# Kernel optimization log

Hardware: AMD Instinct MI355X
Metric: run time of the kernel (lower is better)

## Reference

```python
import jax, jax.numpy as jnp
import numpy as np

N = 50000          # atoms (nodes)
NEIGH = 12         # neighbors per atom
N_CRYS = 500       # crystals, 100 atoms each (contiguous)
H_E = 128          # h_fea_edge
H_A = 128          # h_fea_angle
N_CLS = 2
BOND_STEPS, BOND_MIN, BOND_MAX = 40, 0.0, 8.0
ANG_STEPS, ANG_MIN, ANG_MAX = 8, -1.0, 1.0


def _gbf(data, dmin, dmax, steps):
    # Gaussian basis expansion on the last (new) axis
    filters = jnp.linspace(dmin, dmax, steps, dtype=jnp.float32)
    gamma = (dmax - dmin) / steps
    return jnp.exp(-((data[..., None] - filters) ** 2) / (gamma ** 2))


def _sage_conv(x, src, dst, Wl, Wr, b):
    # PyG SAGEConv, mean aggregation:
    #   out_i = Wl @ mean_{(j->i) in E} x_j + b + Wr @ x_i
    n = x.shape[0]
    msg = x[src]                                             # [E, F] gather
    agg = jax.ops.segment_sum(msg, dst, num_segments=n)      # [N, F] scatter-add
    cnt = jax.ops.segment_sum(jnp.ones((src.shape[0],), x.dtype), dst, num_segments=n)
    agg = agg / jnp.maximum(cnt, 1.0)[:, None]
    return agg @ Wl.T + b + x @ Wr.T


def _segment_mean_pool(x, crys_idx):
    # crys_idx: [C, 2] contiguous [start, end) ranges covering [0, N)
    n = x.shape[0]
    starts = crys_idx[:, 0]
    seg_id = jnp.searchsorted(starts, jnp.arange(n), side='right') - 1
    counts = (crys_idx[:, 1] - crys_idx[:, 0]).astype(x.dtype)
    summed = jax.ops.segment_sum(x, seg_id, num_segments=crys_idx.shape[0])
    return summed / jnp.maximum(counts, 1.0)[:, None]


def setup_inputs() -> dict:
    key = jax.random.key(0)
    ks = jax.random.split(key, 24)
    in_b = BOND_STEPS * NEIGH            # 480
    in_a = ANG_STEPS * NEIGH * NEIGH     # 1152
    h_cat = H_E + H_A                    # 256

    def lin(k, fo, fi):
        return jax.random.normal(k, (fo, fi), jnp.float32) * (1.0 / np.sqrt(fi))

    atoms_per = N // N_CRYS
    starts = np.arange(N_CRYS, dtype=np.int32) * atoms_per
    crys_idx = jnp.asarray(np.stack([starts, starts + atoms_per], axis=1))

    return {
        'bond_fea': jax.random.uniform(ks[0], (N, NEIGH), jnp.float32) * BOND_MAX,
        'angle_fea': jax.random.uniform(ks[1], (N, NEIGH, NEIGH), jnp.float32) * 2.0 - 1.0,
        'species': jax.random.randint(ks[2], (N,), 0, 100, jnp.int32),
        'nbr_idx': jax.random.randint(ks[3], (N, NEIGH), 0, N, jnp.int32),
        'crys_idx': crys_idx,
        'Wl_b1': lin(ks[4], H_E, in_b), 'Wr_b1': lin(ks[5], H_E, in_b),
        'b_b1': jnp.zeros((H_E,), jnp.float32),
        'Wl_a1': lin(ks[6], H_A, in_a), 'Wr_a1': lin(ks[7], H_A, in_a),
        'b_a1': jnp.zeros((H_A,), jnp.float32),
        'Wl_b': jnp.stack([lin(ks[8], H_E, H_E), lin(ks[9], H_E, H_E)]),
        'Wr_b': jnp.stack([lin(ks[10], H_E, H_E), lin(ks[11], H_E, H_E)]),
        'b_b': jnp.zeros((2, H_E), jnp.float32),
        'Wl_a': jnp.stack([lin(ks[12], H_A, H_A), lin(ks[13], H_A, H_A)]),
        'Wr_a': jnp.stack([lin(ks[14], H_A, H_A), lin(ks[15], H_A, H_A)]),
        'b_a': jnp.zeros((2, H_A), jnp.float32),
        'W_mlp': jnp.stack([lin(ks[16], h_cat, h_cat), lin(ks[17], h_cat, h_cat)]),
        'b_mlp': jnp.zeros((2, h_cat), jnp.float32),
        'W_fc': lin(ks[18], N_CLS, h_cat),
        'b_fc': jnp.zeros((N_CLS,), jnp.float32),
    }


def reference(bond_fea, angle_fea, species, nbr_idx, crys_idx,
              Wl_b1, Wr_b1, b_b1, Wl_a1, Wr_a1, b_a1,
              Wl_b, Wr_b, b_b, Wl_a, Wr_a, b_a,
              W_mlp, b_mlp, W_fc, b_fc):
    n, neigh = nbr_idx.shape
    # get_edge_index: source = repeated node id, dest = neighbor id
    src = jnp.repeat(jnp.arange(n, dtype=nbr_idx.dtype), neigh)   # [N*neigh]
    dst = nbr_idx.reshape(-1)                                     # [N*neigh]

    # GBF expansions, flattened per node
    edge_fea = _gbf(bond_fea, BOND_MIN, BOND_MAX, BOND_STEPS).reshape(n, -1)    # [N, 480]
    ang_fea = _gbf(angle_fea, ANG_MIN, ANG_MAX, ANG_STEPS).reshape(n, -1)       # [N, 1152]

    # first SAGE layers (dropout_prob = 0 -> identity)
    b_out = jax.nn.relu(_sage_conv(edge_fea, src, dst, Wl_b1, Wr_b1, b_b1))
    a_out = jax.nn.relu(_sage_conv(ang_fea, src, dst, Wl_a1, Wr_a1, b_a1))

    # stacked SAGE layers (n_conv - 1 = 2 each)
    for i in range(Wl_b.shape[0]):
        b_out = jax.nn.relu(_sage_conv(b_out, src, dst, Wl_b[i], Wr_b[i], b_b[i]))
    for i in range(Wl_a.shape[0]):
        a_out = jax.nn.relu(_sage_conv(a_out, src, dst, Wl_a[i], Wr_a[i], b_a[i]))

    crys_fea = jnp.concatenate([b_out, a_out], axis=1)   # [N, 256]
    crys_fea = _segment_mean_pool(crys_fea, crys_idx)     # [C, 256]

    for i in range(W_mlp.shape[0]):
        crys_fea = crys_fea @ W_mlp[i].T + b_mlp[i]

    return crys_fea @ W_fc.T + b_fc                       # [C, n_classification]
```

## Files before the change

kernel.cpp:

```cpp
#include <hip/hip_runtime.h>

typedef _Float16 f16;
typedef _Float16 f16x8 __attribute__((ext_vector_type(8)));
typedef float f32x4 __attribute__((ext_vector_type(4)));

#define N_ATOMS 50000
#define NEIGH   12
#define NEDGE   (N_ATOMS * NEIGH)
#define NCRYS   500
#define NBLK    196

template <int MODE, int K>
__global__ __launch_bounds__(512) void gemm1(
    const float* __restrict__ Asrc, const f16* __restrict__ Wcat,
    f16* __restrict__ P, f16* __restrict__ Q, int n) {
  __shared__ __align__(16) f16 As[2][4][128][8];
  const int tid = threadIdx.x;
  const int lane = tid & 63;
  const int wid = tid >> 6;
  const int wr = wid >> 2;
  const int wc = wid & 3;
  const int row0 = blockIdx.x * 128;
  const int r16 = lane & 15;
  const int kb = lane >> 4;

  const int sAkb = tid & 3;
  const int sArow = tid >> 2;
  int arow = row0 + sArow;
  if (arow >= n) arow = n - 1;

  const f16* wb[4];
#pragma unroll
  for (int q = 0; q < 4; ++q)
    wb[q] = Wcat + (size_t)(wc * 64 + q * 16 + r16) * K + kb * 8;

  constexpr float G2I = (MODE == 1) ? 25.0f : 16.0f;
  constexpr float DLT = (MODE == 1) ? (8.0f / 39.0f) : (2.0f / 7.0f);
  constexpr float C1 = 2.0f * G2I * DLT;
  constexpr float C2 = G2I * DLT * DLT;
  const float S = __expf(-2.0f * C2);
  constexpr int RUN = (MODE == 1) ? 4 : 8;

  f32x4 acc[4][4];
#pragma unroll
  for (int m = 0; m < 4; ++m)
#pragma unroll
    for (int q = 0; q < 4; ++q) acc[m][q] = (f32x4)0.f;

  auto stageA = [&](int buf, int t) {
    int kg0 = t * 32 + sAkb * 8;
    int jn, kk0;
    if constexpr (MODE == 1) {
      jn = kg0 / 40;
      kk0 = kg0 - jn * 40;
    } else {
      jn = kg0 >> 3;
      kk0 = 0;
    }
    float d = Asrc[(size_t)arow * (MODE == 1 ? 12 : 144) + jn];
    f16 v[8];
#pragma unroll
    for (int h = 0; h < 8 / RUN; ++h) {
      float f0 = (float)(kk0 + h * RUN) * DLT + (MODE == 2 ? -1.0f : 0.0f);
      float u = d - f0;
      float g = __expf(-G2I * u * u);
      float ratio = __expf(C1 * u - C2);
      v[h * RUN] = (f16)g;
#pragma unroll
      for (int j = 1; j < RUN; ++j) {
        g *= ratio;
        ratio *= S;
        v[h * RUN + j] = (f16)g;
      }
    }
    *(f16x8*)&As[buf][sAkb][sArow][0] = *(const f16x8*)v;
  };

  constexpr int NT = K / 32;
  f16x8 bcur[4], bnxt[4];
  stageA(0, 0);
#pragma unroll
  for (int q = 0; q < 4; ++q) bcur[q] = *(const f16x8*)(wb[q]);
  __syncthreads();
  int buf = 0;
  for (int t = 0; t < NT; ++t) {
    if (t + 1 < NT) {
      stageA(buf ^ 1, t + 1);
#pragma unroll
      for (int q = 0; q < 4; ++q) bnxt[q] = *(const f16x8*)(wb[q] + (t + 1) * 32);
    }
    f16x8 a[4];
#pragma unroll
    for (int m = 0; m < 4; ++m)
      a[m] = *(const f16x8*)&As[buf][kb][wr * 64 + m * 16 + r16][0];
#pragma unroll
    for (int m = 0; m < 4; ++m)
#pragma unroll
      for (int q = 0; q < 4; ++q)
        acc[m][q] =
            __builtin_amdgcn_mfma_f32_16x16x32_f16(a[m], bcur[q], acc[m][q], 0, 0, 0);
    __syncthreads();
#pragma unroll
    for (int q = 0; q < 4; ++q) bcur[q] = bnxt[q];
    buf ^= 1;
  }

  const int crow = (lane >> 4) * 4;
  const int ccol = lane & 15;
  f16* outp = (wc < 2) ? P : Q;
  const int cbase = (wc & 1) * 64;
#pragma unroll
  for (int m = 0; m < 4; ++m) {
#pragma unroll
    for (int r = 0; r < 4; ++r) {
      int row = row0 + wr * 64 + m * 16 + crow + r;
      if (row < n) {
#pragma unroll
        for (int q = 0; q < 4; ++q)
          outp[(size_t)row * 128 + cbase + q * 16 + ccol] = (f16)acc[m][q][r];
      }
    }
  }
}

__global__ __launch_bounds__(256) void gemmL_reg(
    const f16* __restrict__ srcB, const f16* __restrict__ srcA,
    f16* __restrict__ dstB, f16* __restrict__ dstA, const f16* __restrict__ Wall,
    const float* __restrict__ bb, const float* __restrict__ ba, int lidx, int n) {
  const int path = blockIdx.y;
  const f16* src = path ? srcA : srcB;
  f16* dst = path ? dstA : dstB;
  const f16* W = Wall + (size_t)(path * 2 + lidx) * 32768;
  const float* bias = (path ? ba : bb) + lidx * 128;

  const int lane = threadIdx.x & 63;
  const int wid = threadIdx.x >> 6;
  const int wr = wid & 1;
  const int wc = wid >> 1;
  const int row0 = blockIdx.x * 128;
  const int r16 = lane & 15;
  const int kb = lane >> 4;

  int rm[4];
#pragma unroll
  for (int m = 0; m < 4; ++m) {
    int r = row0 + wr * 64 + m * 16 + r16;
    rm[m] = (r < n) ? r : (n - 1);
  }
  const f16* wb[4];
#pragma unroll
  for (int q = 0; q < 4; ++q)
    wb[q] = W + (size_t)(wc * 64 + q * 16 + r16) * 256 + kb * 8;

  f32x4 acc[4][4];
#pragma unroll
  for (int m = 0; m < 4; ++m)
#pragma unroll
    for (int q = 0; q < 4; ++q) acc[m][q] = (f32x4)0.f;

#pragma unroll
  for (int t = 0; t < 8; ++t) {
    f16x8 a[4], b[4];
#pragma unroll
    for (int m = 0; m < 4; ++m)
      a[m] = *(const f16x8*)&src[(size_t)rm[m] * 256 + t * 32 + kb * 8];
#pragma unroll
    for (int q = 0; q < 4; ++q) b[q] = *(const f16x8*)(wb[q] + t * 32);
#pragma unroll
    for (int m = 0; m < 4; ++m)
#pragma unroll
      for (int q = 0; q < 4; ++q)
        acc[m][q] =
            __builtin_amdgcn_mfma_f32_16x16x32_f16(a[m], b[q], acc[m][q], 0, 0, 0);
  }

  const int crow = (lane >> 4) * 4;
  const int ccol = lane & 15;
#pragma unroll
  for (int m = 0; m < 4; ++m) {
#pragma unroll
    for (int r = 0; r < 4; ++r) {
      int row = row0 + wr * 64 + m * 16 + crow + r;
      if (row < n) {
#pragma unroll
        for (int q = 0; q < 4; ++q) {
          int col = wc * 64 + q * 16 + ccol;
          float v = acc[m][q][r] + bias[col];
          dst[(size_t)row * 256 + 128 + col] = (f16)fmaxf(v, 0.0f);
        }
      }
    }
  }
}

__global__ void cvtW(const float* __restrict__ Wl, const float* __restrict__ Wr,
                     f16* __restrict__ outp, int K) {
  int c = blockIdx.y;
  int k = blockIdx.x * 256 + threadIdx.x;
  if (k < K)
    outp[(size_t)c * K + k] =
        (f16)((c < 128) ? Wl[(size_t)c * K + k] : Wr[(size_t)(c - 128) * K + k]);
}

__global__ void cvtW_small(const float* __restrict__ Wl_b, const float* __restrict__ Wr_b,
                           const float* __restrict__ Wl_a, const float* __restrict__ Wr_a,
                           f16* __restrict__ outp) {
  int idx = blockIdx.x * 256 + threadIdx.x;
  int l = idx >> 15;
  int c = (idx >> 8) & 127;
  int k = idx & 255;
  const float* Wl = (l < 2) ? Wl_b + (size_t)l * 16384 : Wl_a + (size_t)(l - 2) * 16384;
  const float* Wr = (l < 2) ? Wr_b + (size_t)l * 16384 : Wr_a + (size_t)(l - 2) * 16384;
  float v = (k < 128) ? Wl[(size_t)c * 128 + k] : Wr[(size_t)c * 128 + (k - 128)];
  outp[idx] = (f16)v;
}

__global__ void k_count(const int* __restrict__ nbr, int* __restrict__ deg) {
  int e = blockIdx.x * 256 + threadIdx.x;
  if (e < NEDGE) atomicAdd(&deg[nbr[e]], 1);
}
__global__ void k_scan1(const int* __restrict__ deg, int* __restrict__ rowptr,
                        int* __restrict__ bsum) {
  __shared__ int s[256];
  int t = threadIdx.x, i = blockIdx.x * 256 + t;
  int v = (i < N_ATOMS) ? deg[i] : 0;
  s[t] = v;
  __syncthreads();
  for (int off = 1; off < 256; off <<= 1) {
    int x = (t >= off) ? s[t - off] : 0;
    __syncthreads();
    s[t] += x;
    __syncthreads();
  }
  if (i < N_ATOMS) rowptr[i] = s[t] - v;
  if (t == 255) bsum[blockIdx.x] = s[255];
}
__global__ void k_scan2(int* __restrict__ bsum) {
  __shared__ int s[256];
  int t = threadIdx.x;
  int v = (t < NBLK) ? bsum[t] : 0;
  s[t] = v;
  __syncthreads();
  for (int off = 1; off < 256; off <<= 1) {
    int x = (t >= off) ? s[t - off] : 0;
    __syncthreads();
    s[t] += x;
    __syncthreads();
  }
  if (t < NBLK) bsum[t] = s[t] - v;
}
__global__ void k_scan3(int* __restrict__ rowptr, const int* __restrict__ bsum) {
  int i = blockIdx.x * 256 + threadIdx.x;
  if (i < N_ATOMS) rowptr[i] += bsum[blockIdx.x];
  if (i == 0) rowptr[N_ATOMS] = NEDGE;
}
__global__ void k_fill(const int* __restrict__ nbr, const int* __restrict__ rowptr,
                       int* __restrict__ cursor, int* __restrict__ eidx) {
  int e = blockIdx.x * 256 + threadIdx.x;
  if (e < NEDGE) {
    int dst = nbr[e];
    int pos = rowptr[dst] + atomicAdd(&cursor[dst], 1);
    eidx[pos] = e / NEIGH;
  }
}

__global__ __launch_bounds__(256) void gather_fin1(
    const f16* __restrict__ Pb, const f16* __restrict__ Qb,
    const f16* __restrict__ Pa, const f16* __restrict__ Qa,
    const int* __restrict__ rowptr, const int* __restrict__ eidx,
    const float* __restrict__ bias_b, const float* __restrict__ bias_a,
    f16* __restrict__ axb, f16* __restrict__ axa) {
  const int path = blockIdx.y;
  const f16* P = path ? Pa : Pb;
  const f16* Q = path ? Qa : Qb;
  const float* bias = path ? bias_a : bias_b;
  f16* ax = path ? axa : axb;
  const int t = threadIdx.x;
  const int a = blockIdx.x * 16 + (t >> 4);
  const int g = (t & 15) * 8;
  const int s0 = rowptr[a], s1 = rowptr[a + 1];
  float acc[8];
#pragma unroll
  for (int u = 0; u < 8; ++u) acc[u] = 0.f;
  int j = s0;
  for (; j + 8 <= s1; j += 8) {
    int e[8];
#pragma unroll
    for (int u = 0; u < 8; ++u) e[u] = eidx[j + u];
    f16x8 v[8];
#pragma unroll
    for (int u = 0; u < 8; ++u) v[u] = *(const f16x8*)&P[(size_t)e[u] * 128 + g];
#pragma unroll
    for (int u = 0; u < 8; ++u)
#pragma unroll
      for (int c = 0; c < 8; ++c) acc[c] += (float)v[u][c];
  }
  for (; j + 4 <= s1; j += 4) {
    int e0 = eidx[j], e1 = eidx[j + 1], e2 = eidx[j + 2], e3 = eidx[j + 3];
    f16x8 v0 = *(const f16x8*)&P[(size_t)e0 * 128 + g];
    f16x8 v1 = *(const f16x8*)&P[(size_t)e1 * 128 + g];
    f16x8 v2 = *(const f16x8*)&P[(size_t)e2 * 128 + g];
    f16x8 v3 = *(const f16x8*)&P[(size_t)e3 * 128 + g];
#pragma unroll
    for (int c = 0; c < 8; ++c)
      acc[c] += ((float)v0[c] + (float)v1[c]) + ((float)v2[c] + (float)v3[c]);
  }
  for (; j < s1; ++j) {
    f16x8 v = *(const f16x8*)&P[(size_t)eidx[j] * 128 + g];
#pragma unroll
    for (int c = 0; c < 8; ++c) acc[c] += (float)v[c];
  }
  f16x8 q = *(const f16x8*)&Q[(size_t)a * 128 + g];
  float inv = 1.0f / fmaxf((float)(s1 - s0), 1.0f);
  f16 outv[8];
#pragma unroll
  for (int u = 0; u < 8; ++u) {
    float v = acc[u] * inv + bias[g + u] + (float)q[u];
    outv[u] = (f16)fmaxf(v, 0.0f);
  }
  *(f16x8*)&ax[(size_t)a * 256 + 128 + g] = *(const f16x8*)outv;
}

__global__ __launch_bounds__(256) void gather_mean(
    f16* __restrict__ axb, f16* __restrict__ axa,
    const int* __restrict__ rowptr, const int* __restrict__ eidx) {
  f16* ax = blockIdx.y ? axa : axb;
  const int t = threadIdx.x;
  const int a = blockIdx.x * 16 + (t >> 4);
  const int g = (t & 15) * 8;
  const int s0 = rowptr[a], s1 = rowptr[a + 1];
  float acc[8];
#pragma unroll
  for (int u = 0; u < 8; ++u) acc[u] = 0.f;
  int j = s0;
  for (; j + 8 <= s1; j += 8) {
    int e[8];
#pragma unroll
    for (int u = 0; u < 8; ++u) e[u] = eidx[j + u];
    f16x8 v[8];
#pragma unroll
    for (int u = 0; u < 8; ++u)
      v[u] = *(const f16x8*)&ax[(size_t)e[u] * 256 + 128 + g];
#pragma unroll
    for (int u = 0; u < 8; ++u)
#pragma unroll
      for (int c = 0; c < 8; ++c) acc[c] += (float)v[u][c];
  }
  for (; j + 4 <= s1; j += 4) {
    int e0 = eidx[j], e1 = eidx[j + 1], e2 = eidx[j + 2], e3 = eidx[j + 3];
    f16x8 v0 = *(const f16x8*)&ax[(size_t)e0 * 256 + 128 + g];
    f16x8 v1 = *(const f16x8*)&ax[(size_t)e1 * 256 + 128 + g];
    f16x8 v2 = *(const f16x8*)&ax[(size_t)e2 * 256 + 128 + g];
    f16x8 v3 = *(const f16x8*)&ax[(size_t)e3 * 256 + 128 + g];
#pragma unroll
    for (int c = 0; c < 8; ++c)
      acc[c] += ((float)v0[c] + (float)v1[c]) + ((float)v2[c] + (float)v3[c]);
  }
  for (; j < s1; ++j) {
    f16x8 v = *(const f16x8*)&ax[(size_t)eidx[j] * 256 + 128 + g];
#pragma unroll
    for (int c = 0; c < 8; ++c) acc[c] += (float)v[c];
  }
  float inv = 1.0f / fmaxf((float)(s1 - s0), 1.0f);
  f16 outv[8];
#pragma unroll
  for (int u = 0; u < 8; ++u) outv[u] = (f16)(acc[u] * inv);
  *(f16x8*)&ax[(size_t)a * 256 + g] = *(const f16x8*)outv;
}

__global__ __launch_bounds__(256) void head_kernel(
    const f16* __restrict__ axb, const f16* __restrict__ axa,
    const int* __restrict__ crys, const float* __restrict__ W_mlp,
    const float* __restrict__ b_mlp, const float* __restrict__ W_fc,
    const float* __restrict__ b_fc, float* __restrict__ outp) {
  __shared__ float sh0[256], sh1[256];
  const int cry = blockIdx.x, c = threadIdx.x;
  const int s = crys[2 * cry], e = crys[2 * cry + 1];
  const f16* src = (c < 128) ? axb : axa;
  const int ch = c & 127;
  float sum = 0.f;
  for (int r = s; r < e; ++r) sum += (float)src[(size_t)r * 256 + 128 + ch];
  sh0[c] = sum / fmaxf((float)(e - s), 1.0f);
  __syncthreads();
  {
    const float* wrow = W_mlp + (size_t)c * 256;
    float s2 = b_mlp[c];
#pragma unroll 8
    for (int k = 0; k < 256; k += 4) {
      float4 w = *(const float4*)&wrow[k];
      s2 += sh0[k] * w.x + sh0[k + 1] * w.y + sh0[k + 2] * w.z + sh0[k + 3] * w.w;
    }
    sh1[c] = s2;
  }
  __syncthreads();
  {
    const float* wrow = W_mlp + 65536 + (size_t)c * 256;
    float s2 = b_mlp[256 + c];
#pragma unroll 8
    for (int k = 0; k < 256; k += 4) {
      float4 w = *(const float4*)&wrow[k];
      s2 += sh1[k] * w.x + sh1[k + 1] * w.y + sh1[k + 2] * w.z + sh1[k + 3] * w.w;
    }
    sh0[c] = s2;
  }
  __syncthreads();
  if (c < 2) {
    const float* wrow = W_fc + c * 256;
    float s2 = b_fc[c];
    for (int k = 0; k < 256; ++k) s2 += sh0[k] * wrow[k];
    outp[cry * 2 + c] = s2;
  }
}

extern "C" void kernel_launch(void* const* d_in, const int* in_sizes, int n_in,
                              void* d_out, int out_size, void* d_ws, size_t ws_size,
                              hipStream_t stream) {
  const float* bond  = (const float*)d_in[0];
  const float* angle = (const float*)d_in[1];
  const int*   nbr   = (const int*)d_in[3];
  const int*   crys  = (const int*)d_in[4];
  const float* Wl_b1 = (const float*)d_in[5];
  const float* Wr_b1 = (const float*)d_in[6];
  const float* b_b1  = (const float*)d_in[7];
  const float* Wl_a1 = (const float*)d_in[8];
  const float* Wr_a1 = (const float*)d_in[9];
  const float* b_a1  = (const float*)d_in[10];
  const float* Wl_b  = (const float*)d_in[11];
  const float* Wr_b  = (const float*)d_in[12];
  const float* b_b   = (const float*)d_in[13];
  const float* Wl_a  = (const float*)d_in[14];
  const float* Wr_a  = (const float*)d_in[15];
  const float* b_a   = (const float*)d_in[16];
  const float* W_mlp = (const float*)d_in[17];
  const float* b_mlp = (const float*)d_in[18];
  const float* W_fc  = (const float*)d_in[19];
  const float* b_fc  = (const float*)d_in[20];

  char* w = (char*)d_ws;
  auto alloc = [&](size_t bytes) {
    void* p = (void*)w;
    w += (bytes + 255) & ~(size_t)255;
    return p;
  };
  f16* axbA = (f16*)alloc((size_t)N_ATOMS * 256 * 2);
  f16* axaA = (f16*)alloc((size_t)N_ATOMS * 256 * 2);
  f16* axbB = (f16*)alloc((size_t)N_ATOMS * 256 * 2);
  f16* axaB = (f16*)alloc((size_t)N_ATOMS * 256 * 2);
  f16* Pb = axbB;
  f16* Qb = axbB + (size_t)N_ATOMS * 128;
  f16* Pa = axaB;
  f16* Qa = axaB + (size_t)N_ATOMS * 128;
  f16* Wb1c = (f16*)alloc((size_t)256 * 480 * 2);
  f16* Wa1c = (f16*)alloc((size_t)256 * 1152 * 2);
  f16* Wsm  = (f16*)alloc((size_t)4 * 128 * 256 * 2);
  int* deg    = (int*)alloc((size_t)2 * N_ATOMS * 4);
  int* cursor = deg + N_ATOMS;
  int* rowptr = (int*)alloc((size_t)(N_ATOMS + 1) * 4);
  int* eidx   = (int*)alloc((size_t)NEDGE * 4);
  int* bsum   = (int*)alloc(256 * 4);

  cvtW<<<dim3(2, 256), 256, 0, stream>>>(Wl_b1, Wr_b1, Wb1c, 480);
  cvtW<<<dim3(5, 256), 256, 0, stream>>>(Wl_a1, Wr_a1, Wa1c, 1152);
  cvtW_small<<<512, 256, 0, stream>>>(Wl_b, Wr_b, Wl_a, Wr_a, Wsm);

  hipMemsetAsync(deg, 0, (size_t)2 * N_ATOMS * 4, stream);
  k_count<<<(NEDGE + 255) / 256, 256, 0, stream>>>(nbr, deg);
  k_scan1<<<NBLK, 256, 0, stream>>>(deg, rowptr, bsum);
  k_scan2<<<1, 256, 0, stream>>>(bsum);
  k_scan3<<<NBLK, 256, 0, stream>>>(rowptr, bsum);
  k_fill<<<(NEDGE + 255) / 256, 256, 0, stream>>>(nbr, rowptr, cursor, eidx);

  const int GG = (N_ATOMS + 127) / 128;
  const int AG = N_ATOMS / 16;

  gemm1<2, 1152><<<GG, 512, 0, stream>>>(angle, Wa1c, Pa, Qa, N_ATOMS);
  gemm1<1, 480><<<GG, 512, 0, stream>>>(bond, Wb1c, Pb, Qb, N_ATOMS);
  gather_fin1<<<dim3(AG, 2), 256, 0, stream>>>(Pb, Qb, Pa, Qa, rowptr, eidx,
                                               b_b1, b_a1, axbA, axaA);

  gather_mean<<<dim3(AG, 2), 256, 0, stream>>>(axbA, axaA, rowptr, eidx);
  gemmL_reg<<<dim3(GG, 2), 256, 0, stream>>>(axbA, axaA, axbB, axaB, Wsm, b_b, b_a,
                                             0, N_ATOMS);
  gather_mean<<<dim3(AG, 2), 256, 0, stream>>>(axbB, axaB, rowptr, eidx);
  gemmL_reg<<<dim3(GG, 2), 256, 0, stream>>>(axbB, axaB, axbA, axaA, Wsm, b_b, b_a,
                                             1, N_ATOMS);

  head_kernel<<<NCRYS, 256, 0, stream>>>(axbA, axaA, crys, W_mlp, b_mlp, W_fc, b_fc,
                                         (float*)d_out);
}
```

Baseline: 451.8 us.

## Stage raw input rows in LDS panel and shrink first-layer GEMM tile to 64 rows

The first-layer GEMM now preloads each block's raw bond or angle input rows into a shared-memory panel with vectorized float4 loads. The Gaussian expansion reads from this panel instead of issuing scattered scalar global loads every k-step. The tile shrinks from 128 rows with 8 waves to 64 rows with 4 waves, each wave covering the full 64 rows and a 64-column slice. This gives twice as many blocks but halves weight reuse per block, and the angle panel adds about 37 KB of LDS, which may limit occupancy.

```diff
diff --git a/kernel.cpp b/kernel.cpp
--- a/kernel.cpp
+++ b/kernel.cpp
@@ -11,28 +11,34 @@
 #define NBLK    196
 
 template <int MODE, int K>
-__global__ __launch_bounds__(512) void gemm1(
+__global__ __launch_bounds__(256) void gemm1(
     const float* __restrict__ Asrc, const f16* __restrict__ Wcat,
     f16* __restrict__ P, f16* __restrict__ Q, int n) {
-  __shared__ __align__(16) f16 As[2][4][128][8];
+  constexpr int CIN = (MODE == 1) ? 12 : 144;
+  __shared__ float panel[64][CIN + 1];
+  __shared__ __align__(16) f16 As[2][4][64][8];
   const int tid = threadIdx.x;
   const int lane = tid & 63;
   const int wid = tid >> 6;
-  const int wr = wid >> 2;
-  const int wc = wid & 3;
-  const int row0 = blockIdx.x * 128;
+  const int row0 = blockIdx.x * 64;
   const int r16 = lane & 15;
   const int kb = lane >> 4;
 
-  const int sAkb = tid & 3;
-  const int sArow = tid >> 2;
-  int arow = row0 + sArow;
-  if (arow >= n) arow = n - 1;
+  for (int idx = tid; idx < 64 * (CIN / 4); idx += 256) {
+    int r = idx / (CIN / 4), c4 = idx - r * (CIN / 4);
+    int row = row0 + r;
+    if (row >= n) row = n - 1;
+    float4 v = *(const float4*)&Asrc[(size_t)row * CIN + c4 * 4];
+    panel[r][c4 * 4 + 0] = v.x;
+    panel[r][c4 * 4 + 1] = v.y;
+    panel[r][c4 * 4 + 2] = v.z;
+    panel[r][c4 * 4 + 3] = v.w;
+  }
 
   const f16* wb[4];
 #pragma unroll
   for (int q = 0; q < 4; ++q)
-    wb[q] = Wcat + (size_t)(wc * 64 + q * 16 + r16) * K + kb * 8;
+    wb[q] = Wcat + (size_t)(wid * 64 + q * 16 + r16) * K + kb * 8;
 
   constexpr float G2I = (MODE == 1) ? 25.0f : 16.0f;
   constexpr float DLT = (MODE == 1) ? (8.0f / 39.0f) : (2.0f / 7.0f);
@@ -40,6 +46,9 @@
   constexpr float C2 = G2I * DLT * DLT;
   const float S = __expf(-2.0f * C2);
   constexpr int RUN = (MODE == 1) ? 4 : 8;
+
+  const int sArow = tid & 63;
+  const int sAkb = tid >> 6;
 
   f32x4 acc[4][4];
 #pragma unroll
@@ -57,7 +66,7 @@
       jn = kg0 >> 3;
       kk0 = 0;
     }
-    float d = Asrc[(size_t)arow * (MODE == 1 ? 12 : 144) + jn];
+    float d = panel[sArow][jn];
     f16 v[8];
 #pragma unroll
     for (int h = 0; h < 8 / RUN; ++h) {
@@ -78,6 +87,7 @@
 
   constexpr int NT = K / 32;
   f16x8 bcur[4], bnxt[4];
+  __syncthreads();
   stageA(0, 0);
 #pragma unroll
   for (int q = 0; q < 4; ++q) bcur[q] = *(const f16x8*)(wb[q]);
@@ -92,7 +102,7 @@
     f16x8 a[4];
 #pragma unroll
     for (int m = 0; m < 4; ++m)
-      a[m] = *(const f16x8*)&As[buf][kb][wr * 64 + m * 16 + r16][0];
+      a[m] = *(const f16x8*)&As[buf][kb][m * 16 + r16][0];
 #pragma unroll
     for (int m = 0; m < 4; ++m)
 #pragma unroll
@@ -107,13 +117,13 @@
 
   const int crow = (lane >> 4) * 4;
   const int ccol = lane & 15;
-  f16* outp = (wc < 2) ? P : Q;
-  const int cbase = (wc & 1) * 64;
+  f16* outp = (wid < 2) ? P : Q;
+  const int cbase = (wid & 1) * 64;
 #pragma unroll
   for (int m = 0; m < 4; ++m) {
 #pragma unroll
     for (int r = 0; r < 4; ++r) {
-      int row = row0 + wr * 64 + m * 16 + crow + r;
+      int row = row0 + m * 16 + crow + r;
       if (row < n) {
 #pragma unroll
         for (int q = 0; q < 4; ++q)
@@ -470,20 +480,21 @@
   k_scan3<<<NBLK, 256, 0, stream>>>(rowptr, bsum);
   k_fill<<<(NEDGE + 255) / 256, 256, 0, stream>>>(nbr, rowptr, cursor, eidx);
 
-  const int GG = (N_ATOMS + 127) / 128;
+  const int GG1 = (N_ATOMS + 63) / 64;
+  const int GGL = (N_ATOMS + 127) / 128;
   const int AG = N_ATOMS / 16;
 
-  gemm1<2, 1152><<<GG, 512, 0, stream>>>(angle, Wa1c, Pa, Qa, N_ATOMS);
-  gemm1<1, 480><<<GG, 512, 0, stream>>>(bond, Wb1c, Pb, Qb, N_ATOMS);
+  gemm1<2, 1152><<<GG1, 256, 0, stream>>>(angle, Wa1c, Pa, Qa, N_ATOMS);
+  gemm1<1, 480><<<GG1, 256, 0, stream>>>(bond, Wb1c, Pb, Qb, N_ATOMS);
   gather_fin1<<<dim3(AG, 2), 256, 0, stream>>>(Pb, Qb, Pa, Qa, rowptr, eidx,
                                                b_b1, b_a1, axbA, axaA);
 
   gather_mean<<<dim3(AG, 2), 256, 0, stream>>>(axbA, axaA, rowptr, eidx);
-  gemmL_reg<<<dim3(GG, 2), 256, 0, stream>>>(axbA, axaA, axbB, axaB, Wsm, b_b, b_a,
-                                             0, N_ATOMS);
+  gemmL_reg<<<dim3(GGL, 2), 256, 0, stream>>>(axbA, axaA, axbB, axaB, Wsm, b_b, b_a,
+                                              0, N_ATOMS);
   gather_mean<<<dim3(AG, 2), 256, 0, stream>>>(axbB, axaB, rowptr, eidx);
-  gemmL_reg<<<dim3(GG, 2), 256, 0, stream>>>(axbB, axaB, axbA, axaA, Wsm, b_b, b_a,
-                                             1, N_ATOMS);
+  gemmL_reg<<<dim3(GGL, 2), 256, 0, stream>>>(axbB, axaB, axbA, axaA, Wsm, b_b, b_a,
+                                              1, N_ATOMS);
 
   head_kernel<<<NCRYS, 256, 0, stream>>>(axbA, axaA, crys, W_mlp, b_mlp, W_fc, b_fc,
                                          (float*)d_out);
```

After: 454.5 us. About the same (+0.6%).

## Generate GBF A-fragments in registers and merge both first-layer GEMMs into one launch

Applied to the files above, without the earlier changes.

The first-layer GEMM no longer stages the Gaussian-expanded A tile through shared memory with block-wide barriers. Each wave now computes its own A fragments directly in registers, software-pipelines the scalar input and weight loads, and covers a 64x128 output tile with 256-thread blocks instead of 512. The angle and bond GEMMs are fused into one launch with blockIdx.y choosing the mode, which removes a launch and lets the two run concurrently. In exchange, exp work is duplicated across waves that share rows, and the larger 4x8 accumulator raises register pressure.

```diff
diff --git a/kernel.cpp b/kernel.cpp
--- a/kernel.cpp
+++ b/kernel.cpp
@@ -11,116 +11,131 @@
 #define NBLK    196
 
 template <int MODE, int K>
-__global__ __launch_bounds__(512) void gemm1(
+__device__ __forceinline__ void gemm1_body(
     const float* __restrict__ Asrc, const f16* __restrict__ Wcat,
     f16* __restrict__ P, f16* __restrict__ Q, int n) {
-  __shared__ __align__(16) f16 As[2][4][128][8];
-  const int tid = threadIdx.x;
-  const int lane = tid & 63;
-  const int wid = tid >> 6;
-  const int wr = wid >> 2;
-  const int wc = wid & 3;
-  const int row0 = blockIdx.x * 128;
-  const int r16 = lane & 15;
-  const int kb = lane >> 4;
-
-  const int sAkb = tid & 3;
-  const int sArow = tid >> 2;
-  int arow = row0 + sArow;
-  if (arow >= n) arow = n - 1;
-
-  const f16* wb[4];
-#pragma unroll
-  for (int q = 0; q < 4; ++q)
-    wb[q] = Wcat + (size_t)(wc * 64 + q * 16 + r16) * K + kb * 8;
-
+  constexpr int CIN = (MODE == 1) ? 12 : 144;
+  constexpr int NT = K / 32;
   constexpr float G2I = (MODE == 1) ? 25.0f : 16.0f;
   constexpr float DLT = (MODE == 1) ? (8.0f / 39.0f) : (2.0f / 7.0f);
   constexpr float C1 = 2.0f * G2I * DLT;
   constexpr float C2 = G2I * DLT * DLT;
+  constexpr int RUN = (MODE == 1) ? 4 : 8;
   const float S = __expf(-2.0f * C2);
-  constexpr int RUN = (MODE == 1) ? 4 : 8;
-
-  f32x4 acc[4][4];
+
+  const int lane = threadIdx.x & 63;
+  const int wid = threadIdx.x >> 6;
+  const int wr = wid & 1;
+  const int wc = wid >> 1;
+  const int row0 = blockIdx.x * 128 + wr * 64;
+  const int r16 = lane & 15;
+  const int kb = lane >> 4;
+
+  int rm[4];
+#pragma unroll
+  for (int m = 0; m < 4; ++m) {
+    int r = row0 + m * 16 + r16;
+    rm[m] = (r < n) ? r : (n - 1);
+  }
+  const f16* wbase = Wcat + (size_t)(wc * 128 + r16) * K + kb * 8;
+
+  f32x4 acc[4][8];
 #pragma unroll
   for (int m = 0; m < 4; ++m)
 #pragma unroll
-    for (int q = 0; q < 4; ++q) acc[m][q] = (f32x4)0.f;
-
-  auto stageA = [&](int buf, int t) {
-    int kg0 = t * 32 + sAkb * 8;
-    int jn, kk0;
-    if constexpr (MODE == 1) {
-      jn = kg0 / 40;
-      kk0 = kg0 - jn * 40;
-    } else {
-      jn = kg0 >> 3;
-      kk0 = 0;
+    for (int q = 0; q < 8; ++q) acc[m][q] = (f32x4)0.f;
+
+  auto dload = [&](int t, float* dd) {
+    int kg = t * 32 + kb * 8;
+    int jn = (MODE == 1) ? kg / 40 : (kg >> 3);
+#pragma unroll
+    for (int m = 0; m < 4; ++m) dd[m] = Asrc[(size_t)rm[m] * CIN + jn];
+  };
+  auto bload = [&](int t, f16x8* bb) {
+#pragma unroll
+    for (int q = 0; q < 8; ++q)
+      bb[q] = *(const f16x8*)(wbase + (size_t)q * 16 * K + t * 32);
+  };
+
+  float dA[4], dB[4], dC[4];
+  f16x8 bA[8], bB[8];
+  dload(0, dA);
+  bload(0, bA);
+  if (NT > 1) dload(1, dB);
+
+  for (int t = 0; t < NT; ++t) {
+    if (t + 1 < NT) bload(t + 1, bB);
+    if (t + 2 < NT) dload(t + 2, dC);
+    int kg0 = t * 32 + kb * 8;
+    f16x8 a[4];
+#pragma unroll
+    for (int m = 0; m < 4; ++m) {
+      float d = dA[m];
+      int kk0;
+      if constexpr (MODE == 1) {
+        int jn = kg0 / 40;
+        kk0 = kg0 - jn * 40;
+      } else {
+        kk0 = 0;
+      }
+      f16 v[8];
+#pragma unroll
+      for (int h = 0; h < 8 / RUN; ++h) {
+        float f0 = (float)(kk0 + h * RUN) * DLT + (MODE == 2 ? -1.0f : 0.0f);
+        float u = d - f0;
+        float g = __expf(-G2I * u * u);
+        float ratio = __expf(C1 * u - C2);
+        v[h * RUN] = (f16)g;
+#pragma unroll
+        for (int j = 1; j < RUN; ++j) {
+          g *= ratio;
+          ratio *= S;
+          v[h * RUN + j] = (f16)g;
+        }
+      }
+      a[m] = *(const f16x8*)v;
     }
-    float d = Asrc[(size_t)arow * (MODE == 1 ? 12 : 144) + jn];
-    f16 v[8];
-#pragma unroll
-    for (int h = 0; h < 8 / RUN; ++h) {
-      float f0 = (float)(kk0 + h * RUN) * DLT + (MODE == 2 ? -1.0f : 0.0f);
-      float u = d - f0;
-      float g = __expf(-G2I * u * u);
-      float ratio = __expf(C1 * u - C2);
-      v[h * RUN] = (f16)g;
-#pragma unroll
-      for (int j = 1; j < RUN; ++j) {
-        g *= ratio;
-        ratio *= S;
-        v[h * RUN + j] = (f16)g;
+#pragma unroll
+    for (int m = 0; m < 4; ++m)
+#pragma unroll
+      for (int q = 0; q < 8; ++q)
+        acc[m][q] =
+            __builtin_amdgcn_mfma_f32_16x16x32_f16(a[m], bA[q], acc[m][q], 0, 0, 0);
+#pragma unroll
+    for (int m = 0; m < 4; ++m) {
+      dA[m] = dB[m];
+      dB[m] = dC[m];
+    }
+#pragma unroll
+    for (int q = 0; q < 8; ++q) bA[q] = bB[q];
+  }
+
+  const int crow = (lane >> 4) * 4;
+  const int ccol = lane & 15;
+  f16* outp = wc ? Q : P;
+#pragma unroll
+  for (int m = 0; m < 4; ++m) {
+#pragma unroll
+    for (int r = 0; r < 4; ++r) {
+      int row = row0 + m * 16 + crow + r;
+      if (row < n) {
+#pragma unroll
+        for (int q = 0; q < 8; ++q)
+          outp[(size_t)row * 128 + q * 16 + ccol] = (f16)acc[m][q][r];
       }
     }
-    *(f16x8*)&As[buf][sAkb][sArow][0] = *(const f16x8*)v;
-  };
-
-  constexpr int NT = K / 32;
-  f16x8 bcur[4], bnxt[4];
-  stageA(0, 0);
-#pragma unroll
-  for (int q = 0; q < 4; ++q) bcur[q] = *(const f16x8*)(wb[q]);
-  __syncthreads();
-  int buf = 0;
-  for (int t = 0; t < NT; ++t) {
-    if (t + 1 < NT) {
-      stageA(buf ^ 1, t + 1);
-#pragma unroll
-      for (int q = 0; q < 4; ++q) bnxt[q] = *(const f16x8*)(wb[q] + (t + 1) * 32);
-    }
-    f16x8 a[4];
-#pragma unroll
-    for (int m = 0; m < 4; ++m)
-      a[m] = *(const f16x8*)&As[buf][kb][wr * 64 + m * 16 + r16][0];
-#pragma unroll
-    for (int m = 0; m < 4; ++m)
-#pragma unroll
-      for (int q = 0; q < 4; ++q)
-        acc[m][q] =
-            __builtin_amdgcn_mfma_f32_16x16x32_f16(a[m], bcur[q], acc[m][q], 0, 0, 0);
-    __syncthreads();
-#pragma unroll
-    for (int q = 0; q < 4; ++q) bcur[q] = bnxt[q];
-    buf ^= 1;
-  }
-
-  const int crow = (lane >> 4) * 4;
-  const int ccol = lane & 15;
-  f16* outp = (wc < 2) ? P : Q;
-  const int cbase = (wc & 1) * 64;
-#pragma unroll
-  for (int m = 0; m < 4; ++m) {
-#pragma unroll
-    for (int r = 0; r < 4; ++r) {
-      int row = row0 + wr * 64 + m * 16 + crow + r;
-      if (row < n) {
-#pragma unroll
-        for (int q = 0; q < 4; ++q)
-          outp[(size_t)row * 128 + cbase + q * 16 + ccol] = (f16)acc[m][q][r];
-      }
-    }
-  }
+  }
+}
+
+__global__ __launch_bounds__(256) void gemm1w(
+    const float* __restrict__ angle, const f16* __restrict__ Wa,
+    f16* __restrict__ Pa, f16* __restrict__ Qa,
+    const float* __restrict__ bond, const f16* __restrict__ Wb,
+    f16* __restrict__ Pb, f16* __restrict__ Qb, int n) {
+  if (blockIdx.y == 0)
+    gemm1_body<2, 1152>(angle, Wa, Pa, Qa, n);
+  else
+    gemm1_body<1, 480>(bond, Wb, Pb, Qb, n);
 }
 
 __global__ __launch_bounds__(256) void gemmL_reg(
@@ -473,8 +488,8 @@
   const int GG = (N_ATOMS + 127) / 128;
   const int AG = N_ATOMS / 16;
 
-  gemm1<2, 1152><<<GG, 512, 0, stream>>>(angle, Wa1c, Pa, Qa, N_ATOMS);
-  gemm1<1, 480><<<GG, 512, 0, stream>>>(bond, Wb1c, Pb, Qb, N_ATOMS);
+  gemm1w<<<dim3(GG, 2), 256, 0, stream>>>(angle, Wa1c, Pa, Qa,
+                                          bond, Wb1c, Pb, Qb, N_ATOMS);
   gather_fin1<<<dim3(AG, 2), 256, 0, stream>>>(Pb, Qb, Pa, Qa, rowptr, eidx,
                                                b_b1, b_a1, axbA, axaA);
 
```

After: 463.8 us. 2.6% more time.
